# Optimization experiments

Measured on AMD Instinct MI355X. Metric: run time of the kernel, lower is better.

## Reference

```python
import jax, jax.numpy as jnp
import numpy as np

HIDDEN = 2048
N_HEADS = 16
N_KV = 4
HEAD_DIM = 128
B, T = 2, 2048


def setup_inputs() -> dict:
    key = jax.random.key(0)
    k1, k2, k3, k4 = jax.random.split(key, 4)
    x = jax.random.normal(k1, (B, T, HIDDEN), dtype=jnp.float32)
    # linear weights stored [out, in] like torch; we apply x @ W.T
    w_q = jax.random.normal(k2, (N_HEADS * HEAD_DIM, HIDDEN), dtype=jnp.float32) * (HIDDEN ** -0.5)
    w_kv = jax.random.normal(k3, (2 * N_KV * HEAD_DIM, HIDDEN), dtype=jnp.float32) * (HIDDEN ** -0.5)
    w_o = jax.random.normal(k4, (HIDDEN, N_HEADS * HEAD_DIM), dtype=jnp.float32) * ((N_HEADS * HEAD_DIM) ** -0.5)
    return {"x": x, "w_q": w_q, "w_kv": w_kv, "w_o": w_o}


def reference(x, w_q, w_kv, w_o):
    b, t, _ = x.shape
    groups = N_HEADS // N_KV
    scale = HEAD_DIM ** -0.5

    q = (x @ w_q.T).reshape(b, t, N_HEADS, HEAD_DIM).transpose(0, 2, 1, 3)  # [B,H,T,D]
    kv = x @ w_kv.T
    k, v = jnp.split(kv, 2, axis=-1)
    k = k.reshape(b, t, N_KV, HEAD_DIM).transpose(0, 2, 1, 3)  # [B,KV,T,D]
    v = v.reshape(b, t, N_KV, HEAD_DIM).transpose(0, 2, 1, 3)
    # repeat_interleave over head dim -> [B,H,T,D]
    k = jnp.repeat(k, groups, axis=1)
    v = jnp.repeat(v, groups, axis=1)

    scores = jnp.einsum('bhqd,bhkd->bhqk', q, k) * scale  # [B,H,T,T]
    causal = jnp.triu(jnp.ones((t, t), dtype=bool), k=1)
    scores = jnp.where(causal, -jnp.inf, scores)
    weights = jax.nn.softmax(scores, axis=-1)
    out = jnp.einsum('bhqk,bhkd->bhqd', weights, v)  # [B,H,T,D]
    out = out.transpose(0, 2, 1, 3).reshape(b, t, N_HEADS * HEAD_DIM)
    return out @ w_o.T
```

## Files before the change

### kernel.cpp

```cpp
#include <hip/hip_runtime.h>

typedef short bf16x8 __attribute__((ext_vector_type(8)));
typedef float f32x4 __attribute__((ext_vector_type(4)));
typedef unsigned int u32x4 __attribute__((ext_vector_type(4)));

__device__ __forceinline__ unsigned short f2bf(float f) {
    unsigned int u = __float_as_uint(f);
    u = (u + 0x7fff + ((u >> 16) & 1)) >> 16;
    return (unsigned short)u;
}
__device__ __forceinline__ float bf2f(short s) {
    return __uint_as_float(((unsigned int)(unsigned short)s) << 16);
}

__device__ __forceinline__ void async16(const void* g, void* l) {
    __builtin_amdgcn_global_load_lds(
        (const __attribute__((address_space(1))) void*)g,
        (__attribute__((address_space(3))) void*)l,
        16 , 0 , 0 );
}

__global__ void castk(const float* __restrict__ in, unsigned short* __restrict__ out, int n4) {
    int i = blockIdx.x * blockDim.x + threadIdx.x;
    if (i < n4) {
        float4 f = ((const float4*)in)[i];
        ushort4 u;
        u.x = f2bf(f.x); u.y = f2bf(f.y); u.z = f2bf(f.z); u.w = f2bf(f.w);
        ((ushort4*)out)[i] = u;
    }
}

template <int NREP, typename OutT>
__global__ __launch_bounds__(512, 2) void gemm8p(const unsigned short* __restrict__ A,
                                                 const unsigned short* __restrict__ B,
                                                 OutT* __restrict__ C,
                                                 int N, int K, int NT,
                                                 int ncut, float qscale) {
    constexpr int NCH = 4 + NREP;
    __shared__ __attribute__((aligned(16))) unsigned short LA[2][256 * 64];
    __shared__ __attribute__((aligned(16))) unsigned short LB[2][NREP * 64 * 64];

    const int tid  = threadIdx.x;
    const int lane = tid & 63;
    const int w    = tid >> 6;
    const int quad = lane >> 4;
    const int l16  = lane & 15;
    const int wm   = w >> 2;
    const int wn   = w & 3;
    const int m0   = blockIdx.x * 256;
    const int n0   = blockIdx.y * (NREP * 64);
    const int swz  = (l16 & 7) << 3;

    const int lr = lane >> 3;
    const int ls = lane & 7;
    const int ss = ls ^ lr;
    const unsigned short* aSrc = A + (size_t)(m0 + w * 8 + lr) * K + ss * 8;
    const unsigned short* bSrc = B + (size_t)(n0 + w * 8 + lr) * K + ss * 8;

    f32x4 acc[8][NREP] = {};

    auto stage1 = [&](int nb, int t, int si) {
        if (si >= NCH) return;
        if (si < NREP) {
            async16(bSrc + (size_t)si * 64 * K + t * 64, &LB[nb][(si * 64 + w * 8) * 64]);
        } else {
            int j = si - NREP;
            int c = (j == 0) ? 0 : (j == 1) ? 2 : (j == 2) ? 1 : 3;
            async16(aSrc + (size_t)c * 64 * K + t * 64, &LA[nb][(c * 64 + w * 8) * 64]);
        }
    };

    auto phase = [&](int cur, int q, bf16x8 (&bf)[NREP][2], int tn, bool last) {
        bf16x8 af[2][2];
        if (q == 0) {
#pragma unroll
            for (int n = 0; n < NREP; ++n)
#pragma unroll
                for (int kk = 0; kk < 2; ++kk)
                    bf[n][kk] = *(const bf16x8*)&LB[cur][(size_t)(wn * (NREP * 16) + n * 16 + l16) * 64
                                                         + ((kk * 32 + quad * 8) ^ swz)];
        }
#pragma unroll
        for (int mi = 0; mi < 2; ++mi)
#pragma unroll
            for (int kk = 0; kk < 2; ++kk)
                af[mi][kk] = *(const bf16x8*)&LA[cur][(size_t)(wm * 128 + (q * 2 + mi) * 16 + l16) * 64
                                                      + ((kk * 32 + quad * 8) ^ swz)];
        if (!last) { stage1(cur ^ 1, tn, 2 * q); stage1(cur ^ 1, tn, 2 * q + 1); }
        if (q == 1) {
            if (last) asm volatile("s_waitcnt vmcnt(0)" ::: "memory");
            else      asm volatile("s_waitcnt vmcnt(4)" ::: "memory");
        }
        if (q == 3 && !last) asm volatile("s_waitcnt vmcnt(2)" ::: "memory");
        __builtin_amdgcn_s_barrier();
        asm volatile("s_waitcnt lgkmcnt(0)" ::: "memory");
        __builtin_amdgcn_sched_barrier(0);
        __builtin_amdgcn_s_setprio(1);
#pragma unroll
        for (int mi = 0; mi < 2; ++mi)
#pragma unroll
            for (int n = 0; n < NREP; ++n)
#pragma unroll
                for (int kk = 0; kk < 2; ++kk)
                    acc[q * 2 + mi][n] = __builtin_amdgcn_mfma_f32_16x16x32_bf16(
                        af[mi][kk], bf[n][kk], acc[q * 2 + mi][n], 0, 0, 0);
        __builtin_amdgcn_s_setprio(0);
        __builtin_amdgcn_s_barrier();
    };

    auto ktile = [&](int cur, int tn, bool last) {
        bf16x8 bf[NREP][2];
        phase(cur, 0, bf, tn, last);
        phase(cur, 1, bf, tn, last);
        phase(cur, 2, bf, tn, last);
        phase(cur, 3, bf, tn, last);
    };

#pragma unroll
    for (int s = 0; s < NCH; ++s) stage1(0, 0, s);
    asm volatile("s_waitcnt vmcnt(2)" ::: "memory");
    __builtin_amdgcn_s_barrier();

    int cur = 0;
    for (int t = 0; t < NT - 1; ++t) {
        ktile(cur, t + 1, false);
        cur ^= 1;
    }
    ktile(cur, 0, true);

#pragma unroll
    for (int m = 0; m < 8; ++m) {
        int row = m0 + wm * 128 + m * 16 + quad * 4;
#pragma unroll
        for (int n = 0; n < NREP; ++n) {
            int col = n0 + wn * (NREP * 16) + n * 16 + l16;
            f32x4 v = acc[m][n];
            float s = (col < ncut) ? qscale : 1.0f;
#pragma unroll
            for (int j = 0; j < 4; ++j) {
                float vj = v[j] * s;
                if constexpr (sizeof(OutT) == 4)
                    C[(size_t)(row + j) * N + col] = vj;
                else
                    C[(size_t)(row + j) * N + col] = f2bf(vj);
            }
        }
    }
}

__global__ __launch_bounds__(256) void transpose_v(const unsigned short* __restrict__ QKV,
                                                   unsigned short* __restrict__ Vt) {
    __shared__ unsigned short Ls[64 * 136];
    const int tid = threadIdx.x;
    const int k0  = blockIdx.x * 64;
    const int b   = blockIdx.y >> 2;
    const int kvh = blockIdx.y & 3;

#pragma unroll
    for (int pass = 0; pass < 4; ++pass) {
        int c = tid + pass * 256;
        int key = c >> 4, dc = (c & 15) * 8;
        bf16x8 v = *(const bf16x8*)(QKV + (size_t)(b * 2048 + k0 + key) * 3072 + 2560 + kvh * 128 + dc);
        *(bf16x8*)&Ls[key * 136 + dc] = v;
    }
    __syncthreads();
#pragma unroll
    for (int pass = 0; pass < 4; ++pass) {
        int c = tid + pass * 256;
        int d = c >> 3, kc = (c & 7) * 8;
        bf16x8 v;
#pragma unroll
        for (int i = 0; i < 8; ++i) v[i] = (short)Ls[(kc + i) * 136 + d];
        *(bf16x8*)(Vt + ((size_t)(b * 4 + kvh) * 128 + d) * 2048 + k0 + kc) = v;
    }
}

__global__ __launch_bounds__(256, 2) void attn_fwd6(const unsigned short* __restrict__ QKV,
                                                    const unsigned short* __restrict__ Vt,
                                                    unsigned short* __restrict__ Opart,
                                                    float* __restrict__ lpart) {
    __shared__ __attribute__((aligned(16))) unsigned short Ks[2][64 * 128];
    __shared__ __attribute__((aligned(16))) unsigned short Vs[2][128 * 64];

    const int tid  = threadIdx.x;
    const int lane = tid & 63;
    const int w    = tid >> 6;
    const int quad = lane >> 4;
    const int l16  = lane & 15;
    const int swz  = (l16 & 7) << 3;

    const int hb   = blockIdx.x;
    const int h    = hb & 15;
    const int b    = hb >> 4;
    const int y    = blockIdx.y;
    const int p    = 15 - (y >> 1);
    const int half = y & 1;
    const int kvh  = h >> 2;
    const float M_FIX = 12.0f;

    const int ntot   = p + 1;
    const int tstart = half ? ntot : 0;
    const int tend   = half ? 2 * ntot : ntot;

    const int qbase = p * 128;
    const int qw0   = qbase + w * 32;
    const int qw1   = qw0 + 16;

    bf16x8 qf[2][4];
#pragma unroll
    for (int g = 0; g < 2; ++g)
#pragma unroll
        for (int kd = 0; kd < 4; ++kd)
            qf[g][kd] = *(const bf16x8*)(QKV + (size_t)(b * 2048 + qw0 + g * 16 + l16) * 3072
                                         + h * 128 + kd * 32 + quad * 8);

    f32x4 oacc[2][8] = {};
    float rs[2] = {0.f, 0.f};

    const unsigned short* gk[4];
    const unsigned short* gv[4];
#pragma unroll
    for (int pp = 0; pp < 4; ++pp) {
        int r  = (4 * w + pp) * 4 + (lane >> 4);
        int s  = lane & 15;
        int sp = (s & 8) | ((s ^ r) & 7);
        gk[pp] = QKV + (size_t)(b * 2048 + r) * 3072 + 2048 + kvh * 128 + sp * 8;
        int d  = (4 * w + pp) * 8 + (lane >> 3);
        int sv = (lane & 7) ^ (d & 7);
        gv[pp] = Vt + ((size_t)(b * 4 + kvh) * 128 + d) * 2048 + sv * 8;
    }

    auto stage = [&](int nb, int t) {
        const size_t ko = (size_t)t * 64;
#pragma unroll
        for (int pp = 0; pp < 4; ++pp) {
            async16(gk[pp] + ko * 3072, &Ks[nb][(4 * w + pp) * 512]);
            async16(gv[pp] + ko,        &Vs[nb][(4 * w + pp) * 512]);
        }
    };

    const int  srcA = l16 + ((lane & 16) << 1);
    const int  srcB = srcA + 16;
    const bool hiq  = (lane & 32) != 0;

    stage(0, tstart);
    int cur = 0;

    for (int t = tstart; t < tend; ++t) {
        __syncthreads();
        if (t + 1 < tend) stage(cur ^ 1, t + 1);
        const int k0 = t * 64;

        if (k0 <= qw0 + 15) {
            const bool live1 = (k0 <= qw1 + 15);

            f32x4 sacc[2][4] = {};
            __builtin_amdgcn_s_setprio(1);
#pragma unroll
            for (int kt = 0; kt < 4; ++kt) {
                bf16x8 kf[4];
#pragma unroll
                for (int kd = 0; kd < 4; ++kd)
                    kf[kd] = *(const bf16x8*)&Ks[cur][(kt * 16 + l16) * 128
                                                      + ((kd * 32 + quad * 8) ^ swz)];
#pragma unroll
                for (int kd = 0; kd < 4; ++kd)
                    sacc[0][kt] = __builtin_amdgcn_mfma_f32_16x16x32_bf16(kf[kd], qf[0][kd], sacc[0][kt], 0, 0, 0);
                if (live1) {
#pragma unroll
                    for (int kd = 0; kd < 4; ++kd)
                        sacc[1][kt] = __builtin_amdgcn_mfma_f32_16x16x32_bf16(kf[kd], qf[1][kd], sacc[1][kt], 0, 0, 0);
                }
            }
            __builtin_amdgcn_s_setprio(0);

            bf16x8 pa[2][2];
#pragma unroll
            for (int g = 0; g < 2; ++g) {
                if (g == 1 && !live1) continue;
                const int qwg  = qw0 + g * 16;
                const bool diag = (k0 + 63 > qwg);
                const int qrow = qwg + l16;
                unsigned int pk[4][2];
#pragma unroll
                for (int kt = 0; kt < 4; ++kt) {
                    float pvv[4];
#pragma unroll
                    for (int j = 0; j < 4; ++j) {
                        float pv = __expf(sacc[g][kt][j] - M_FIX);
                        if (diag) {
                            int key = k0 + kt * 16 + quad * 4 + j;
                            if (key > qrow) pv = 0.f;
                        }
                        rs[g] += pv;
                        pvv[j] = pv;
                    }
                    asm("v_cvt_pk_bf16_f32 %0, %1, %2" : "=v"(pk[kt][0]) : "v"(pvv[0]), "v"(pvv[1]));
                    asm("v_cvt_pk_bf16_f32 %0, %1, %2" : "=v"(pk[kt][1]) : "v"(pvv[2]), "v"(pvv[3]));
                }
#pragma unroll
                for (int ks = 0; ks < 2; ++ks) {
                    unsigned int a0 = __shfl(pk[2 * ks][0],     srcA, 64);
                    unsigned int b0 = __shfl(pk[2 * ks + 1][0], srcA, 64);
                    unsigned int a1 = __shfl(pk[2 * ks][1],     srcA, 64);
                    unsigned int b1 = __shfl(pk[2 * ks + 1][1], srcA, 64);
                    unsigned int a2 = __shfl(pk[2 * ks][0],     srcB, 64);
                    unsigned int b2 = __shfl(pk[2 * ks + 1][0], srcB, 64);
                    unsigned int a3 = __shfl(pk[2 * ks][1],     srcB, 64);
                    unsigned int b3 = __shfl(pk[2 * ks + 1][1], srcB, 64);
                    u32x4 tt;
                    tt.x = hiq ? b0 : a0;
                    tt.y = hiq ? b1 : a1;
                    tt.z = hiq ? b2 : a2;
                    tt.w = hiq ? b3 : a3;
                    pa[g][ks] = __builtin_bit_cast(bf16x8, tt);
                }
            }

            __builtin_amdgcn_s_setprio(1);
#pragma unroll
            for (int dt = 0; dt < 8; ++dt) {
                bf16x8 vf[2];
#pragma unroll
                for (int ks = 0; ks < 2; ++ks)
                    vf[ks] = *(const bf16x8*)&Vs[cur][(dt * 16 + l16) * 64
                                                      + ((ks * 32 + quad * 8) ^ swz)];
#pragma unroll
                for (int ks = 0; ks < 2; ++ks)
                    oacc[0][dt] = __builtin_amdgcn_mfma_f32_16x16x32_bf16(pa[0][ks], vf[ks], oacc[0][dt], 0, 0, 0);
                if (live1) {
#pragma unroll
                    for (int ks = 0; ks < 2; ++ks)
                        oacc[1][dt] = __builtin_amdgcn_mfma_f32_16x16x32_bf16(pa[1][ks], vf[ks], oacc[1][dt], 0, 0, 0);
                }
            }
            __builtin_amdgcn_s_setprio(0);
        }
        cur ^= 1;
    }

#pragma unroll
    for (int g = 0; g < 2; ++g) {
        float r = rs[g];
        r += __shfl_xor(r, 16, 64);
        r += __shfl_xor(r, 32, 64);
        if (lane < 16)
            lpart[((size_t)(half * 2 + b) * 16 + h) * 2048 + qw0 + g * 16 + lane] = r;
#pragma unroll
        for (int dt = 0; dt < 8; ++dt)
#pragma unroll
            for (int j = 0; j < 4; ++j) {
                int qrow = qw0 + g * 16 + quad * 4 + j;
                Opart[(size_t)(half * 4096 + b * 2048 + qrow) * 2048 + h * 128 + dt * 16 + l16] =
                    f2bf(oacc[g][dt][j]);
            }
    }
}

__global__ __launch_bounds__(256) void combine(const unsigned short* __restrict__ Opart,
                                               const float* __restrict__ lpart,
                                               unsigned short* __restrict__ O) {
    const int r   = blockIdx.x;
    const int b   = r >> 11, row = r & 2047;
    const int col = threadIdx.x * 8;
    const int h   = col >> 7;
    bf16x8 a = *(const bf16x8*)(Opart + (size_t)r * 2048 + col);
    bf16x8 c = *(const bf16x8*)(Opart + (size_t)(4096 + r) * 2048 + col);
    float la = lpart[((size_t)(0 * 2 + b) * 16 + h) * 2048 + row];
    float lb = lpart[((size_t)(1 * 2 + b) * 16 + h) * 2048 + row];
    float inv = 1.0f / (la + lb);
    bf16x8 o;
#pragma unroll
    for (int i = 0; i < 8; ++i)
        o[i] = (short)f2bf((bf2f(a[i]) + bf2f(c[i])) * inv);
    *(bf16x8*)(O + (size_t)r * 2048 + col) = o;
}

extern "C" void kernel_launch(void* const* d_in, const int* in_sizes, int n_in,
                              void* d_out, int out_size, void* d_ws, size_t ws_size,
                              hipStream_t stream) {
    const float* x   = (const float*)d_in[0];
    const float* wq  = (const float*)d_in[1];
    const float* wkv = (const float*)d_in[2];
    const float* wo  = (const float*)d_in[3];
    float* out = (float*)d_out;

    char* ws = (char*)d_ws;
    size_t off = 0;
    auto alloc = [&](size_t bytes) { size_t o = off; off += (bytes + 255) & ~(size_t)255; return o; };
    unsigned short* xb    = (unsigned short*)(ws + alloc((size_t)4096 * 2048 * 2));
    unsigned short* wqkvb = (unsigned short*)(ws + alloc((size_t)3072 * 2048 * 2));
    unsigned short* wob   = (unsigned short*)(ws + alloc((size_t)2048 * 2048 * 2));
    unsigned short* QKVb  = (unsigned short*)(ws + alloc((size_t)4096 * 3072 * 2));
    unsigned short* Ab    = (unsigned short*)(ws + alloc((size_t)4096 * 2048 * 2));
    unsigned short* Vtb   = (unsigned short*)(ws + alloc((size_t)2 * 4 * 128 * 2048 * 2));
    unsigned short* Opart = (unsigned short*)(ws + alloc((size_t)2 * 4096 * 2048 * 2));
    float*          lpart = (float*)(ws + alloc((size_t)2 * 2 * 16 * 2048 * 4));

    const float qscale = 0.08838834764831845f;

    castk<<<8192, 256, 0, stream>>>(x,   xb,    4096 * 2048 / 4);
    castk<<<4096, 256, 0, stream>>>(wq,  wqkvb, 2048 * 2048 / 4);
    castk<<<2048, 256, 0, stream>>>(wkv, wqkvb + (size_t)2048 * 2048, 1024 * 2048 / 4);
    castk<<<4096, 256, 0, stream>>>(wo,  wob,   2048 * 2048 / 4);

    gemm8p<3, unsigned short><<<dim3(16, 16), 512, 0, stream>>>(xb, wqkvb, QKVb, 3072, 2048, 32, 2048, qscale);

    transpose_v<<<dim3(32, 8), 256, 0, stream>>>(QKVb, Vtb);

    attn_fwd6<<<dim3(32, 32), 256, 0, stream>>>(QKVb, Vtb, Opart, lpart);
    combine<<<4096, 256, 0, stream>>>(Opart, lpart, Ab);

    gemm8p<2, float><<<dim3(16, 16), 512, 0, stream>>>(Ab, wob, out, 2048, 2048, 32, 0, 1.0f);
}
```

Baseline: 289.3 us.

## Fuse casts, write transposed V from QKV GEMM, single-buffer K in attention

Merges the four cast launches into one kernel and has the QKV GEMM epilogue write the V block directly in transposed layout, which removes the separate transpose kernel. The attention kernel keeps only one K buffer in shared memory, loading the next K tile after a second barrier once scores are computed, so it can run at 3 blocks per CU. The trade is an extra barrier per tile and less overlap for the K load, in exchange for higher occupancy and fewer launches.

```diff
diff --git a/kernel.cpp b/kernel.cpp
--- a/kernel.cpp
+++ b/kernel.cpp
@@ -20,20 +20,30 @@
         16 , 0 , 0 );
 }
 
-__global__ void castk(const float* __restrict__ in, unsigned short* __restrict__ out, int n4) {
+__global__ __launch_bounds__(256) void castall(const float* __restrict__ x,
+                                               const float* __restrict__ wq,
+                                               const float* __restrict__ wkv,
+                                               const float* __restrict__ wo,
+                                               unsigned short* __restrict__ xb,
+                                               unsigned short* __restrict__ wqkvb,
+                                               unsigned short* __restrict__ wob) {
     int i = blockIdx.x * blockDim.x + threadIdx.x;
-    if (i < n4) {
-        float4 f = ((const float4*)in)[i];
-        ushort4 u;
-        u.x = f2bf(f.x); u.y = f2bf(f.y); u.z = f2bf(f.z); u.w = f2bf(f.w);
-        ((ushort4*)out)[i] = u;
-    }
+    const float* src; unsigned short* dst; int j;
+    if (i < 2097152)      { src = x;   dst = xb;    j = i; }
+    else if (i < 3145728) { src = wq;  dst = wqkvb; j = i - 2097152; }
+    else if (i < 3670016) { src = wkv; dst = wqkvb + (size_t)2048 * 2048; j = i - 3145728; }
+    else                  { src = wo;  dst = wob;   j = i - 3670016; }
+    float4 f = ((const float4*)src)[j];
+    ushort4 u;
+    u.x = f2bf(f.x); u.y = f2bf(f.y); u.z = f2bf(f.z); u.w = f2bf(f.w);
+    ((ushort4*)dst)[j] = u;
 }
 
 template <int NREP, typename OutT>
 __global__ __launch_bounds__(512, 2) void gemm8p(const unsigned short* __restrict__ A,
                                                  const unsigned short* __restrict__ B,
                                                  OutT* __restrict__ C,
+                                                 unsigned short* __restrict__ VtOut,
                                                  int N, int K, int NT,
                                                  int ncut, float qscale) {
     constexpr int NCH = 4 + NREP;
@@ -136,50 +146,30 @@
             int col = n0 + wn * (NREP * 16) + n * 16 + l16;
             f32x4 v = acc[m][n];
             float s = (col < ncut) ? qscale : 1.0f;
-#pragma unroll
-            for (int j = 0; j < 4; ++j) {
-                float vj = v[j] * s;
-                if constexpr (sizeof(OutT) == 4)
-                    C[(size_t)(row + j) * N + col] = vj;
-                else
-                    C[(size_t)(row + j) * N + col] = f2bf(vj);
+            if (VtOut != nullptr && col >= 2560) {
+                int bb = row >> 11, t0 = row & 2047;
+                ushort4 o;
+                o.x = f2bf(v[0]); o.y = f2bf(v[1]); o.z = f2bf(v[2]); o.w = f2bf(v[3]);
+                *(ushort4*)(VtOut + ((size_t)(bb * 512 + (col - 2560))) * 2048 + t0) = o;
+            } else {
+#pragma unroll
+                for (int j = 0; j < 4; ++j) {
+                    float vj = v[j] * s;
+                    if constexpr (sizeof(OutT) == 4)
+                        C[(size_t)(row + j) * N + col] = vj;
+                    else
+                        C[(size_t)(row + j) * N + col] = f2bf(vj);
+                }
             }
         }
     }
 }
 
-__global__ __launch_bounds__(256) void transpose_v(const unsigned short* __restrict__ QKV,
-                                                   unsigned short* __restrict__ Vt) {
-    __shared__ unsigned short Ls[64 * 136];
-    const int tid = threadIdx.x;
-    const int k0  = blockIdx.x * 64;
-    const int b   = blockIdx.y >> 2;
-    const int kvh = blockIdx.y & 3;
-
-#pragma unroll
-    for (int pass = 0; pass < 4; ++pass) {
-        int c = tid + pass * 256;
-        int key = c >> 4, dc = (c & 15) * 8;
-        bf16x8 v = *(const bf16x8*)(QKV + (size_t)(b * 2048 + k0 + key) * 3072 + 2560 + kvh * 128 + dc);
-        *(bf16x8*)&Ls[key * 136 + dc] = v;
-    }
-    __syncthreads();
-#pragma unroll
-    for (int pass = 0; pass < 4; ++pass) {
-        int c = tid + pass * 256;
-        int d = c >> 3, kc = (c & 7) * 8;
-        bf16x8 v;
-#pragma unroll
-        for (int i = 0; i < 8; ++i) v[i] = (short)Ls[(kc + i) * 136 + d];
-        *(bf16x8*)(Vt + ((size_t)(b * 4 + kvh) * 128 + d) * 2048 + k0 + kc) = v;
-    }
-}
-
-__global__ __launch_bounds__(256, 2) void attn_fwd6(const unsigned short* __restrict__ QKV,
+__global__ __launch_bounds__(256, 3) void attn_fwd7(const unsigned short* __restrict__ QKV,
                                                     const unsigned short* __restrict__ Vt,
                                                     unsigned short* __restrict__ Opart,
                                                     float* __restrict__ lpart) {
-    __shared__ __attribute__((aligned(16))) unsigned short Ks[2][64 * 128];
+    __shared__ __attribute__((aligned(16))) unsigned short Ks[64 * 128];
     __shared__ __attribute__((aligned(16))) unsigned short Vs[2][128 * 64];
 
     const int tid  = threadIdx.x;
@@ -230,39 +220,44 @@
         gv[pp] = Vt + ((size_t)(b * 4 + kvh) * 128 + d) * 2048 + sv * 8;
     }
 
-    auto stage = [&](int nb, int t) {
+    auto stageK = [&](int t) {
         const size_t ko = (size_t)t * 64;
 #pragma unroll
-        for (int pp = 0; pp < 4; ++pp) {
-            async16(gk[pp] + ko * 3072, &Ks[nb][(4 * w + pp) * 512]);
-            async16(gv[pp] + ko,        &Vs[nb][(4 * w + pp) * 512]);
-        }
+        for (int pp = 0; pp < 4; ++pp)
+            async16(gk[pp] + ko * 3072, &Ks[(4 * w + pp) * 512]);
+    };
+    auto stageV = [&](int nb, int t) {
+        const size_t ko = (size_t)t * 64;
+#pragma unroll
+        for (int pp = 0; pp < 4; ++pp)
+            async16(gv[pp] + ko, &Vs[nb][(4 * w + pp) * 512]);
     };
 
     const int  srcA = l16 + ((lane & 16) << 1);
     const int  srcB = srcA + 16;
     const bool hiq  = (lane & 32) != 0;
 
-    stage(0, tstart);
+    stageK(tstart);
+    stageV(0, tstart);
     int cur = 0;
 
     for (int t = tstart; t < tend; ++t) {
         __syncthreads();
-        if (t + 1 < tend) stage(cur ^ 1, t + 1);
+        if (t + 1 < tend) stageV(cur ^ 1, t + 1);
         const int k0 = t * 64;
-
-        if (k0 <= qw0 + 15) {
-            const bool live1 = (k0 <= qw1 + 15);
-
-            f32x4 sacc[2][4] = {};
+        const bool liveW = (k0 <= qw0 + 15);
+        const bool live1 = (k0 <= qw1 + 15);
+
+        f32x4 sacc[2][4] = {};
+        if (liveW) {
             __builtin_amdgcn_s_setprio(1);
 #pragma unroll
             for (int kt = 0; kt < 4; ++kt) {
                 bf16x8 kf[4];
 #pragma unroll
                 for (int kd = 0; kd < 4; ++kd)
-                    kf[kd] = *(const bf16x8*)&Ks[cur][(kt * 16 + l16) * 128
-                                                      + ((kd * 32 + quad * 8) ^ swz)];
+                    kf[kd] = *(const bf16x8*)&Ks[(kt * 16 + l16) * 128
+                                                 + ((kd * 32 + quad * 8) ^ swz)];
 #pragma unroll
                 for (int kd = 0; kd < 4; ++kd)
                     sacc[0][kt] = __builtin_amdgcn_mfma_f32_16x16x32_bf16(kf[kd], qf[0][kd], sacc[0][kt], 0, 0, 0);
@@ -273,7 +268,12 @@
                 }
             }
             __builtin_amdgcn_s_setprio(0);
-
+        }
+
+        __syncthreads();
+        if (t + 1 < tend) stageK(t + 1);
+
+        if (liveW) {
             bf16x8 pa[2][2];
 #pragma unroll
             for (int g = 0; g < 2; ++g) {
@@ -399,17 +399,14 @@
 
     const float qscale = 0.08838834764831845f;
 
-    castk<<<8192, 256, 0, stream>>>(x,   xb,    4096 * 2048 / 4);
-    castk<<<4096, 256, 0, stream>>>(wq,  wqkvb, 2048 * 2048 / 4);
-    castk<<<2048, 256, 0, stream>>>(wkv, wqkvb + (size_t)2048 * 2048, 1024 * 2048 / 4);
-    castk<<<4096, 256, 0, stream>>>(wo,  wob,   2048 * 2048 / 4);
-
-    gemm8p<3, unsigned short><<<dim3(16, 16), 512, 0, stream>>>(xb, wqkvb, QKVb, 3072, 2048, 32, 2048, qscale);
-
-    transpose_v<<<dim3(32, 8), 256, 0, stream>>>(QKVb, Vtb);
-
-    attn_fwd6<<<dim3(32, 32), 256, 0, stream>>>(QKVb, Vtb, Opart, lpart);
+    castall<<<18432, 256, 0, stream>>>(x, wq, wkv, wo, xb, wqkvb, wob);
+
+    gemm8p<3, unsigned short><<<dim3(16, 16), 512, 0, stream>>>(xb, wqkvb, QKVb, Vtb,
+                                                                3072, 2048, 32, 2048, qscale);
+
+    attn_fwd7<<<dim3(32, 32), 256, 0, stream>>>(QKVb, Vtb, Opart, lpart);
     combine<<<4096, 256, 0, stream>>>(Opart, lpart, Ab);
 
-    gemm8p<2, float><<<dim3(16, 16), 512, 0, stream>>>(Ab, wob, out, 2048, 2048, 32, 0, 1.0f);
-}
+    gemm8p<2, float><<<dim3(16, 16), 512, 0, stream>>>(Ab, wob, out, nullptr,
+                                                       2048, 2048, 32, 0, 1.0f);
+}
```

Result: slower. 335.4 us (+15.9%).
